# Kernel optimization log

Measured on AMD Instinct MI355X. Metric: run time of the kernel, lower is better.

Reference implementation:

```python
import jax, jax.numpy as jnp
import numpy as np

N, E, F_IN, HID, G, HEADS = 50000, 300000, 128, 256, 1000, 1
NUM_GC, ALPHA = 5, 0.5
EPS_LN = 1e-5
EPS_BN = 1e-5


def _layer_norm(h, g, b):
    m = h.mean(-1, keepdims=True)
    v = jnp.mean((h - m) ** 2, axis=-1, keepdims=True)
    return (h - m) * jax.lax.rsqrt(v + EPS_LN) * g + b


def _l2_normalize_rows(h):
    # F.normalize(h, dim=1)
    n = jnp.sqrt(jnp.sum(h * h, axis=1, keepdims=True))
    return h / jnp.maximum(n, 1e-12)


def full_attention_conv(qs, ks, vs):
    # qs:[N,H,M] ks:[L,H,M] vs:[L,H,D]; global (Frobenius) norm as in torch.norm(p=2)
    qs = qs / jnp.linalg.norm(qs)
    ks = ks / jnp.linalg.norm(ks)
    n = qs.shape[0]
    kvs = jnp.einsum('lhm,lhd->hmd', ks, vs)                 # [H,M,D]
    attn_num = jnp.einsum('nhm,hmd->nhd', qs, kvs) + n * vs  # [N,H,D]
    ks_sum = ks.sum(axis=0)                                  # [H,M]
    norm = jnp.einsum('nhm,hm->nh', qs, ks_sum)[..., None] + n
    return attn_num / norm                                   # [N,H,D]


def setup_inputs() -> dict:
    key = jax.random.key(0)
    ks = jax.random.split(key, 24)
    f32 = jnp.float32

    def lin(k, fan_in, shape):
        return jax.random.normal(k, shape, f32) / np.sqrt(fan_in)

    inp = {}
    inp['x'] = jax.random.normal(ks[0], (N, F_IN), f32)
    inp['edge_index'] = jax.random.randint(ks[1], (2, E), 0, N)
    inp['batch'] = jnp.sort(jax.random.randint(ks[2], (N,), 0, G))
    inp['beta'] = 1
    # TransConv params
    inp['fc_W'] = lin(ks[3], F_IN, (F_IN, HID)); inp['fc_b'] = jnp.zeros((HID,), f32)
    inp['ln0_g'] = jnp.ones((HID,), f32); inp['ln0_b'] = jnp.zeros((HID,), f32)
    inp['Wq'] = lin(ks[4], HID, (HID, HID * HEADS)); inp['bq'] = jnp.zeros((HID * HEADS,), f32)
    inp['Wk'] = lin(ks[5], HID, (HID, HID * HEADS)); inp['bk'] = jnp.zeros((HID * HEADS,), f32)
    inp['Wv'] = lin(ks[6], HID, (HID, HID * HEADS)); inp['bv'] = jnp.zeros((HID * HEADS,), f32)
    inp['ln1_g'] = jnp.ones((HID,), f32); inp['ln1_b'] = jnp.zeros((HID,), f32)
    # GCN stack params
    inp['gcn_W0'] = lin(ks[7], F_IN, (F_IN, HID)); inp['gcn_b0'] = jnp.zeros((HID,), f32)
    inp['gcn_W'] = jnp.stack([lin(ks[8 + i], HID, (HID, HID)) for i in range(NUM_GC - 1)])
    inp['gcn_b'] = jnp.zeros((NUM_GC - 1, HID), f32)
    inp['bn_g'] = jnp.ones((NUM_GC, HID), f32); inp['bn_b'] = jnp.zeros((NUM_GC, HID), f32)
    inp['bn_mean'] = jnp.zeros((NUM_GC, HID), f32); inp['bn_var'] = jnp.ones((NUM_GC, HID), f32)
    return inp


def reference(x, edge_index, batch, beta, fc_W, fc_b, ln0_g, ln0_b,
              Wq, bq, Wk, bk, Wv, bv, ln1_g, ln1_b,
              gcn_W0, gcn_b0, gcn_W, gcn_b, bn_g, bn_b, bn_mean, bn_var):
    n = x.shape[0]
    # ---- TransConv branch (eval mode: dropout = identity) ----
    h = jax.nn.relu(_layer_norm(x @ fc_W + fc_b, ln0_g, ln0_b))
    qs = (h @ Wq + bq).reshape(n, HEADS, HID)
    kk = (h @ Wk + bk).reshape(n, HEADS, HID)
    vv = (h @ Wv + bv).reshape(n, HEADS, HID)
    attn = full_attention_conv(qs, kk, vv).mean(axis=1)      # [N,HID]
    h1 = ALPHA * attn + (1.0 - ALPHA) * h                    # residual
    h1 = jax.nn.relu(_layer_norm(h1, ln1_g, ln1_b))
    x_trans = _l2_normalize_rows(h1)
    # ---- GCN stack ----
    src, dst = edge_index[0], edge_index[1]
    loop = jnp.arange(n)
    src_f = jnp.concatenate([src, loop])
    dst_f = jnp.concatenate([dst, loop])
    deg = jax.ops.segment_sum(jnp.ones_like(src_f, dtype=x.dtype), dst_f, num_segments=n)
    dinv = jax.lax.rsqrt(deg)  # deg >= 1 due to self loops
    enorm = (dinv[src_f] * dinv[dst_f])[:, None]             # [E+N,1]
    g = x
    for i in range(NUM_GC):
        W = gcn_W0 if i == 0 else gcn_W[i - 1]
        b = gcn_b0 if i == 0 else gcn_b[i - 1]
        gw = g @ W
        g = jax.ops.segment_sum(gw[src_f] * enorm, dst_f, num_segments=n) + b
        g = (g - bn_mean[i]) * jax.lax.rsqrt(bn_var[i] + EPS_BN) * bn_g[i] + bn_b[i]
        if i != NUM_GC - 1:
            g = jax.nn.relu(g)
    g = _l2_normalize_rows(g)
    xpool = jax.ops.segment_sum(g, batch, num_segments=G)    # global_add_pool
    return (xpool, g, x_trans)
```

## Files before the change

### kernel.cpp

```cpp
#include <hip/hip_runtime.h>
#include <stdint.h>

#define NN 50000
#define NEDGE 300000
#define FIN 128
#define HID 256
#define NG 1000
#define NLAYER 5

typedef __bf16 bf16x8 __attribute__((ext_vector_type(8)));
typedef float f32x4 __attribute__((ext_vector_type(4)));

__device__ __forceinline__ float us2f(unsigned short u){
  union{ unsigned int i; float f; } c; c.i = ((unsigned int)u) << 16; return c.f;
}
__device__ __forceinline__ unsigned short f2us(float f){
  union{ float f; unsigned int i; } c; c.f = f;
  unsigned int r = c.i + 0x7fff + ((c.i >> 16) & 1);
  return (unsigned short)(r >> 16);
}

__device__ __forceinline__ void gload16(const void* g, void* l){
  __builtin_amdgcn_global_load_lds((__attribute__((address_space(1))) void*)g,
                                   (__attribute__((address_space(3))) void*)l, 16, 0, 0);
}

__device__ __forceinline__ void fma8(float* a, uint4 u, float w){
  a[0] += w * us2f((unsigned short)(u.x & 0xffff));
  a[1] += w * us2f((unsigned short)(u.x >> 16));
  a[2] += w * us2f((unsigned short)(u.y & 0xffff));
  a[3] += w * us2f((unsigned short)(u.y >> 16));
  a[4] += w * us2f((unsigned short)(u.z & 0xffff));
  a[5] += w * us2f((unsigned short)(u.z >> 16));
  a[6] += w * us2f((unsigned short)(u.w & 0xffff));
  a[7] += w * us2f((unsigned short)(u.w >> 16));
}

template<int K, int EPI>
__global__ void gemm_epi(const unsigned short* __restrict__ A,
                         const unsigned short* __restrict__ Wt,
                         const float* __restrict__ bias,
                         const float* __restrict__ p1,
                         const float* __restrict__ p2,
                         const unsigned short* __restrict__ hres,
                         void* __restrict__ outv, int nrows)
{
  __shared__ __align__(16) char smem[20480];
  unsigned short* Alds = (unsigned short*)smem;
  unsigned short* Wlds = (unsigned short*)(smem + 4096);
  const int t = threadIdx.x;
  const int lane = t & 63, w = t >> 6;
  const int r0 = blockIdx.x * 64;

  const int ccl = (t & 3) ^ ((t >> 3) & 3);
  int arow = r0 + (t >> 2); if (arow > nrows - 1) arow = nrows - 1;
  const unsigned short* aSrc = A + (size_t)arow * K + ccl * 8;
  const unsigned short* wSrc[4];
#pragma unroll
  for (int i = 0; i < 4; ++i){
    int c = i * 64 + (t >> 2);
    wSrc[i] = Wt + (size_t)c * K + ccl * 8;
  }

  f32x4 acc[4][4] = {};
  const int lg = lane >> 4, lr = lane & 15;

  for (int k0 = 0; k0 < K; k0 += 32){
    gload16(aSrc + k0, smem + t * 16);
#pragma unroll
    for (int i = 0; i < 4; ++i)
      gload16(wSrc[i] + k0, smem + 4096 + (i * 256 + t) * 16);
    __syncthreads();

    bf16x8 af[4], bfr[4];
#pragma unroll
    for (int mi = 0; mi < 4; ++mi){
      int r = mi * 16 + lr;
      int cp = lg ^ ((r >> 1) & 3);
      af[mi] = *(const bf16x8*)(Alds + (r * 4 + cp) * 8);
    }
#pragma unroll
    for (int ni = 0; ni < 4; ++ni){
      int c = w * 64 + ni * 16 + lr;
      int cp = lg ^ ((c >> 1) & 3);
      bfr[ni] = *(const bf16x8*)(Wlds + (c * 4 + cp) * 8);
    }
#pragma unroll
    for (int mi = 0; mi < 4; ++mi)
#pragma unroll
      for (int ni = 0; ni < 4; ++ni)
        acc[mi][ni] = __builtin_amdgcn_mfma_f32_16x16x32_bf16(af[mi], bfr[ni], acc[mi][ni], 0, 0, 0);
    __syncthreads();
  }

  float g1[4], g2[4], bc[4];
#pragma unroll
  for (int ni = 0; ni < 4; ++ni){
    int c = w * 64 + ni * 16 + lr;
    g1[ni] = p1[c]; g2[ni] = p2[c];
    if (EPI <= 2) bc[ni] = bias[c];
  }

  float* redS = (float*)smem;
  float* redQ = redS + 256;
  float* meanr = redQ + 256;
  float* rstdr = meanr + 64;
  float* invr  = rstdr + 64;

  if (EPI == 1 || EPI == 2){
#pragma unroll
    for (int mi = 0; mi < 4; ++mi)
#pragma unroll
      for (int ni = 0; ni < 4; ++ni)
#pragma unroll
        for (int e = 0; e < 4; ++e){
          float v = acc[mi][ni][e] + bc[ni];
          if (EPI == 2){
            int gr = r0 + mi * 16 + lg * 4 + e; if (gr > nrows - 1) gr = nrows - 1;
            int c = w * 64 + ni * 16 + lr;
            v = 0.5f * v + 0.5f * us2f(hres[(size_t)gr * 256 + c]);
          }
          acc[mi][ni][e] = v;
        }
    float ps[4][4], pq[4][4];
#pragma unroll
    for (int mi = 0; mi < 4; ++mi)
#pragma unroll
      for (int e = 0; e < 4; ++e){
        float s = 0.f, q = 0.f;
#pragma unroll
        for (int ni = 0; ni < 4; ++ni){ float v = acc[mi][ni][e]; s += v; q += v * v; }
        ps[mi][e] = s; pq[mi][e] = q;
      }
#pragma unroll
    for (int m = 1; m <= 8; m <<= 1)
#pragma unroll
      for (int mi = 0; mi < 4; ++mi)
#pragma unroll
        for (int e = 0; e < 4; ++e){
          ps[mi][e] += __shfl_xor(ps[mi][e], m);
          pq[mi][e] += __shfl_xor(pq[mi][e], m);
        }
    if (lr == 0){
#pragma unroll
      for (int mi = 0; mi < 4; ++mi)
#pragma unroll
        for (int e = 0; e < 4; ++e){
          int row = mi * 16 + lg * 4 + e;
          redS[w * 64 + row] = ps[mi][e];
          redQ[w * 64 + row] = pq[mi][e];
        }
    }
    __syncthreads();
    if (t < 64){
      float S = redS[t] + redS[64 + t] + redS[128 + t] + redS[192 + t];
      float Q = redQ[t] + redQ[64 + t] + redQ[128 + t] + redQ[192 + t];
      float mean = S * (1.f / 256.f);
      float var = Q * (1.f / 256.f) - mean * mean;
      meanr[t] = mean; rstdr[t] = rsqrtf(var + 1e-5f);
    }
    __syncthreads();
#pragma unroll
    for (int mi = 0; mi < 4; ++mi)
#pragma unroll
      for (int e = 0; e < 4; ++e){
        int row = mi * 16 + lg * 4 + e;
        float mean = meanr[row], rstd = rstdr[row];
#pragma unroll
        for (int ni = 0; ni < 4; ++ni){
          float y = (acc[mi][ni][e] - mean) * rstd * g1[ni] + g2[ni];
          acc[mi][ni][e] = fmaxf(y, 0.f);
        }
      }
  } else {
#pragma unroll
    for (int mi = 0; mi < 4; ++mi)
#pragma unroll
      for (int ni = 0; ni < 4; ++ni)
#pragma unroll
        for (int e = 0; e < 4; ++e){
          float y = acc[mi][ni][e] * g1[ni] + g2[ni];
          if (EPI == 3) y = fmaxf(y, 0.f);
          acc[mi][ni][e] = y;
        }
  }

  if (EPI == 1 || EPI == 3){
    unsigned short* out = (unsigned short*)outv;
#pragma unroll
    for (int mi = 0; mi < 4; ++mi)
#pragma unroll
      for (int e = 0; e < 4; ++e){
        int gr = r0 + mi * 16 + lg * 4 + e;
        if (gr < nrows){
          unsigned short* orow = out + (size_t)gr * 256 + w * 64 + lr;
#pragma unroll
          for (int ni = 0; ni < 4; ++ni)
            orow[ni * 16] = f2us(acc[mi][ni][e]);
        }
      }
  } else {
    float ps[4][4];
#pragma unroll
    for (int mi = 0; mi < 4; ++mi)
#pragma unroll
      for (int e = 0; e < 4; ++e){
        float s = 0.f;
#pragma unroll
        for (int ni = 0; ni < 4; ++ni){ float v = acc[mi][ni][e]; s += v * v; }
        ps[mi][e] = s;
      }
#pragma unroll
    for (int m = 1; m <= 8; m <<= 1)
#pragma unroll
      for (int mi = 0; mi < 4; ++mi)
#pragma unroll
        for (int e = 0; e < 4; ++e)
          ps[mi][e] += __shfl_xor(ps[mi][e], m);
    __syncthreads();
    if (lr == 0){
#pragma unroll
      for (int mi = 0; mi < 4; ++mi)
#pragma unroll
        for (int e = 0; e < 4; ++e)
          redS[w * 64 + mi * 16 + lg * 4 + e] = ps[mi][e];
    }
    __syncthreads();
    if (t < 64){
      float S = redS[t] + redS[64 + t] + redS[128 + t] + redS[192 + t];
      invr[t] = 1.f / fmaxf(sqrtf(S), 1e-12f);
    }
    __syncthreads();
    float* out = (float*)outv;
#pragma unroll
    for (int mi = 0; mi < 4; ++mi)
#pragma unroll
      for (int e = 0; e < 4; ++e){
        int row = mi * 16 + lg * 4 + e;
        int gr = r0 + row;
        float inv = invr[row];
        if (gr < nrows){
          float* orow = out + (size_t)gr * 256 + w * 64 + lr;
#pragma unroll
          for (int ni = 0; ni < 4; ++ni)
            orow[ni * 16] = acc[mi][ni][e] * inv;
        }
      }
  }
}

__global__ void k_cvt(const float* __restrict__ s, unsigned short* __restrict__ d, int n8){
  int i = blockIdx.x * 256 + threadIdx.x;
  if (i < n8){
    const float4* sp = (const float4*)s + (size_t)i * 2;
    float4 a = sp[0], b = sp[1];
    ushort4 u0, u1;
    u0.x = f2us(a.x); u0.y = f2us(a.y); u0.z = f2us(a.z); u0.w = f2us(a.w);
    u1.x = f2us(b.x); u1.y = f2us(b.y); u1.z = f2us(b.z); u1.w = f2us(b.w);
    ushort4* dp = (ushort4*)d + (size_t)i * 2;
    dp[0] = u0; dp[1] = u1;
  }
}

__global__ void k_wprep(const float* __restrict__ fcW, const float* __restrict__ Wv,
                        const float* __restrict__ gW0, const float* __restrict__ gW,
                        unsigned short* __restrict__ fcWt, unsigned short* __restrict__ WvT,
                        unsigned short* __restrict__ g0T, unsigned short* __restrict__ gWT)
{
  int which = blockIdx.z;
  const float* src; unsigned short* dst; int K;
  if (which == 0){ src = fcW; dst = fcWt; K = FIN; }
  else if (which == 1){ src = Wv; dst = WvT; K = 256; }
  else if (which == 2){ src = gW0; dst = g0T; K = FIN; }
  else { src = gW + (size_t)(which - 3) * 65536; dst = gWT + (size_t)(which - 3) * 65536; K = 256; }
  int bx = blockIdx.x * 64; if (bx >= K) return;
  int by = blockIdx.y * 64;
  __shared__ unsigned short tile[64][65];
  int t = threadIdx.x;
#pragma unroll
  for (int j = 0; j < 16; ++j){
    int idx = j * 256 + t;
    int r = idx >> 6, c = idx & 63;
    tile[r][c] = f2us(src[(size_t)(bx + r) * 256 + by + c]);
  }
  __syncthreads();
#pragma unroll
  for (int j = 0; j < 16; ++j){
    int idx = j * 256 + t;
    int rr = idx >> 6, cc = idx & 63;
    dst[(size_t)(by + rr) * K + bx + cc] = tile[cc][rr];
  }
}

__global__ void k_bnprep(const float* __restrict__ gb0, const float* __restrict__ gb,
                         const float* __restrict__ bng, const float* __restrict__ bnb,
                         const float* __restrict__ bnm, const float* __restrict__ bnv,
                         float* __restrict__ scale, float* __restrict__ shift)
{
  int l = blockIdx.x, c = threadIdx.x;
  int i = l * 256 + c;
  float b = (l == 0) ? gb0[c] : gb[(l - 1) * 256 + c];
  float sc = bng[i] * rsqrtf(bnv[i] + 1e-5f);
  scale[i] = sc;
  shift[i] = (b - bnm[i]) * sc + bnb[i];
}

__global__ void k_deg_init(int* deg){ int i = blockIdx.x * 256 + threadIdx.x; if (i < NN) deg[i] = 1; }
__global__ void k_deg_count(const int* __restrict__ ei, int* deg){
  int e = blockIdx.x * 256 + threadIdx.x;
  if (e < NEDGE) atomicAdd(&deg[ei[NEDGE + e]], 1);
}
__global__ void k_scan_part(const int* __restrict__ deg, int* rp, int* bsum){
  __shared__ int sh[256];
  int t = threadIdx.x, i = blockIdx.x * 256 + t;
  int v = (i < NN) ? deg[i] : 0;
  sh[t] = v; __syncthreads();
  for (int off = 1; off < 256; off <<= 1){
    int x = (t >= off) ? sh[t - off] : 0;
    __syncthreads(); sh[t] += x; __syncthreads();
  }
  if (i < NN) rp[i] = sh[t] - v;
  if (t == 255) bsum[blockIdx.x] = sh[255];
}
__global__ void k_scan_sums(int* rp, int* bsum, int nb){
  __shared__ int sh[256];
  int t = threadIdx.x;
  int v = (t < nb) ? bsum[t] : 0;
  sh[t] = v; __syncthreads();
  for (int off = 1; off < 256; off <<= 1){
    int x = (t >= off) ? sh[t - off] : 0;
    __syncthreads(); sh[t] += x; __syncthreads();
  }
  if (t < nb) bsum[t] = sh[t] - v;
  if (t == 0) rp[NN] = sh[255];
}
__global__ void k_scan_add(int* rp, const int* __restrict__ bsum, const int* __restrict__ deg,
                           int* fill, float* dinv){
  int i = blockIdx.x * 256 + threadIdx.x;
  if (i < NN){
    int r = rp[i] + bsum[i >> 8];
    rp[i] = r; fill[i] = r;
    dinv[i] = rsqrtf((float)deg[i]);
  }
}
__global__ void k_fill_edges(const int* __restrict__ ei, int* fill, int* colx, float* ew,
                             const float* __restrict__ dinv){
  int e = blockIdx.x * 256 + threadIdx.x;
  if (e < NEDGE){
    int s = ei[e], d = ei[NEDGE + e];
    int p = atomicAdd(&fill[d], 1);
    colx[p] = s; ew[p] = dinv[s] * dinv[d];
  }
}
__global__ void k_fill_self(int* fill, int* colx, float* ew, const float* __restrict__ dinv){
  int i = blockIdx.x * 256 + threadIdx.x;
  if (i < NN){
    int p = atomicAdd(&fill[i], 1);
    colx[p] = i; ew[p] = dinv[i] * dinv[i];
  }
}

template<int NC>
__global__ void __launch_bounds__(256) k_aggregate(
    const unsigned short* __restrict__ gsrc, const int* __restrict__ rp,
    const int* __restrict__ colx, const float* __restrict__ ew,
    unsigned short* __restrict__ gout)
{
  constexpr int LG = (NC == 256) ? 5 : 4;
  int tid = blockIdx.x * 256 + threadIdx.x;
  int nd = tid >> LG;
  if (nd >= NN) return;
  int c0 = (tid & ((1 << LG) - 1)) * 8;
  const unsigned short* base = gsrc + c0;
  int jb = rp[nd], je = rp[nd + 1];
  float a0[8] = {}, a1[8] = {};
  int j = jb;
  for (; j + 2 <= je; j += 2){
    int s0 = colx[j], s1 = colx[j + 1];
    float w0 = ew[j], w1 = ew[j + 1];
    uint4 u0 = *(const uint4*)(base + (size_t)s0 * NC);
    uint4 u1 = *(const uint4*)(base + (size_t)s1 * NC);
    fma8(a0, u0, w0);
    fma8(a1, u1, w1);
  }
  if (j < je){
    uint4 u = *(const uint4*)(base + (size_t)colx[j] * NC);
    fma8(a0, u, ew[j]);
  }
  uint4 pk;
  pk.x = (unsigned int)f2us(a0[0] + a1[0]) | ((unsigned int)f2us(a0[1] + a1[1]) << 16);
  pk.y = (unsigned int)f2us(a0[2] + a1[2]) | ((unsigned int)f2us(a0[3] + a1[3]) << 16);
  pk.z = (unsigned int)f2us(a0[4] + a1[4]) | ((unsigned int)f2us(a0[5] + a1[5]) << 16);
  pk.w = (unsigned int)f2us(a0[6] + a1[6]) | ((unsigned int)f2us(a0[7] + a1[7]) << 16);
  *(uint4*)(gout + (size_t)nd * NC + c0) = pk;
}

__global__ void k_gbounds(const int* __restrict__ batch, int* __restrict__ gstart)
{
  int i = blockIdx.x * 256 + threadIdx.x;
  if (i >= NN) return;
  int bc = batch[i];
  int bp = (i == 0) ? -1 : batch[i - 1];
  for (int g = bp + 1; g <= bc; ++g) gstart[g] = i;
  if (i == NN - 1)
    for (int g = bc + 1; g <= NG; ++g) gstart[g] = NN;
}

__global__ void k_pool(const float* __restrict__ out1, const int* __restrict__ gstart,
                       float* __restrict__ out0)
{
  int g = blockIdx.x, c = threadIdx.x;
  int js = gstart[g], je = gstart[g + 1];
  float acc = 0.f;
  int r = js;
  for (; r + 4 <= je; r += 4){
    float a = out1[(size_t)r * 256 + c];
    float b = out1[(size_t)(r + 1) * 256 + c];
    float d = out1[(size_t)(r + 2) * 256 + c];
    float e = out1[(size_t)(r + 3) * 256 + c];
    acc += (a + b) + (d + e);
  }
  for (; r < je; ++r) acc += out1[(size_t)r * 256 + c];
  out0[(size_t)g * 256 + c] = acc;
}

extern "C" void kernel_launch(void* const* d_in, const int* in_sizes, int n_in,
                              void* d_out, int out_size, void* d_ws, size_t ws_size,
                              hipStream_t stream)
{
  const float* x    = (const float*)d_in[0];
  const int*  ei    = (const int*)d_in[1];
  const int*  batch = (const int*)d_in[2];
  const float* fcW  = (const float*)d_in[4];
  const float* fcb  = (const float*)d_in[5];
  const float* ln0g = (const float*)d_in[6];
  const float* ln0b = (const float*)d_in[7];
  const float* Wv   = (const float*)d_in[12];
  const float* bv   = (const float*)d_in[13];
  const float* ln1g = (const float*)d_in[14];
  const float* ln1b = (const float*)d_in[15];
  const float* gW0  = (const float*)d_in[16];
  const float* gb0  = (const float*)d_in[17];
  const float* gW   = (const float*)d_in[18];
  const float* gb   = (const float*)d_in[19];
  const float* bng  = (const float*)d_in[20];
  const float* bnb  = (const float*)d_in[21];
  const float* bnm  = (const float*)d_in[22];
  const float* bnv  = (const float*)d_in[23];

  char* ws = (char*)d_ws;
  unsigned short* xb   = (unsigned short*)(ws);
  unsigned short* hb   = (unsigned short*)(ws + 12800000);
  unsigned short* ga   = (unsigned short*)(ws + 38400000);
  unsigned short* fcWt = (unsigned short*)(ws + 64000000);
  unsigned short* WvT  = (unsigned short*)(ws + 64065536);
  unsigned short* g0T  = (unsigned short*)(ws + 64196608);
  unsigned short* gWT  = (unsigned short*)(ws + 64262144);
  float* bnscale       = (float*)(ws + 64786432);
  float* bnshift       = (float*)(ws + 64791552);
  int*   deg           = (int*)(ws + 64796672);
  int*   rp            = (int*)(ws + 64996672);
  int*   fill          = (int*)(ws + 65196736);
  float* dinv          = (float*)(ws + 65396736);
  int*   colx          = (int*)(ws + 65596736);
  float* ew            = (float*)(ws + 66996736);
  int*   bsum          = (int*)(ws + 68396736);
  int*   gstart        = (int*)(ws + 68397760);

  float* out0 = (float*)d_out;
  float* out1 = out0 + NG * 256;
  float* out2 = out1 + NN * 256;

  k_cvt<<<(NN * FIN / 8 + 255) / 256, 256, 0, stream>>>(x, xb, NN * FIN / 8);
  k_wprep<<<dim3(4, 4, 7), 256, 0, stream>>>(fcW, Wv, gW0, gW, fcWt, WvT, g0T, gWT);
  k_bnprep<<<NLAYER, 256, 0, stream>>>(gb0, gb, bng, bnb, bnm, bnv, bnscale, bnshift);
  k_gbounds<<<196, 256, 0, stream>>>(batch, gstart);

  const int GB = (NN + 63) / 64;
  gemm_epi<FIN, 1><<<GB, 256, 0, stream>>>(xb, fcWt, fcb, ln0g, ln0b, nullptr, hb, NN);
  gemm_epi<256, 2><<<GB, 256, 0, stream>>>(hb, WvT, bv, ln1g, ln1b, hb, out2, NN);

  k_deg_init<<<196, 256, 0, stream>>>(deg);
  k_deg_count<<<(NEDGE + 255) / 256, 256, 0, stream>>>(ei, deg);
  k_scan_part<<<196, 256, 0, stream>>>(deg, rp, bsum);
  k_scan_sums<<<1, 256, 0, stream>>>(rp, bsum, 196);
  k_scan_add<<<196, 256, 0, stream>>>(rp, bsum, deg, fill, dinv);
  k_fill_edges<<<(NEDGE + 255) / 256, 256, 0, stream>>>(ei, fill, colx, ew, dinv);
  k_fill_self<<<196, 256, 0, stream>>>(fill, colx, ew, dinv);

  const int AB128 = (NN * 16 + 255) / 256;
  const int AB256 = (NN * 32 + 255) / 256;
  k_aggregate<128><<<AB128, 256, 0, stream>>>(xb, rp, colx, ew, ga);
  gemm_epi<FIN, 3><<<GB, 256, 0, stream>>>(ga, g0T, nullptr, bnscale, bnshift, nullptr, hb, NN);
  for (int i = 1; i < NLAYER - 1; ++i){
    k_aggregate<256><<<AB256, 256, 0, stream>>>(hb, rp, colx, ew, ga);
    gemm_epi<256, 3><<<GB, 256, 0, stream>>>(ga, gWT + (size_t)(i - 1) * 65536, nullptr,
        bnscale + i * 256, bnshift + i * 256, nullptr, hb, NN);
  }
  k_aggregate<256><<<AB256, 256, 0, stream>>>(hb, rp, colx, ew, ga);
  gemm_epi<256, 4><<<GB, 256, 0, stream>>>(ga, gWT + (size_t)3 * 65536, nullptr,
      bnscale + 4 * 256, bnshift + 4 * 256, nullptr, out1, NN);

  k_pool<<<NG, 256, 0, stream>>>(out1, gstart, out0);
}
```

Measured before the change: 358.2 us.

## Merge preprocessing kernels into one launch and single-block CSR scan

Folds the input conversion, weight transpose, batchnorm folding, graph-bounds and degree-count kernels into one multi-role kernel, replaces the three-kernel prefix scan with a single 1024-thread block, and merges the edge and self-loop fill into one kernel. The degree array is zeroed with a memset and the self-loop +1 is added during the scan. The goal is to cut about ten kernel launches and their serialization gaps. The trade-off is that the single-block scan runs serially over about 49 elements per thread.

```diff
diff --git a/kernel.cpp b/kernel.cpp
--- a/kernel.cpp
+++ b/kernel.cpp
@@ -249,114 +249,129 @@
   }
 }
 
-__global__ void k_cvt(const float* __restrict__ s, unsigned short* __restrict__ d, int n8){
-  int i = blockIdx.x * 256 + threadIdx.x;
-  if (i < n8){
-    const float4* sp = (const float4*)s + (size_t)i * 2;
-    float4 a = sp[0], b = sp[1];
+#define PB_CVT 3125
+#define PB_WP  112
+#define PB_BN  NLAYER
+#define PB_GB  196
+#define PB_DC  1172
+#define PB_TOTAL (PB_CVT + PB_WP + PB_BN + PB_GB + PB_DC)
+
+__global__ void k_pre(const float* __restrict__ x, unsigned short* __restrict__ xb,
+                      const float* __restrict__ fcW, const float* __restrict__ Wv,
+                      const float* __restrict__ gW0, const float* __restrict__ gW,
+                      unsigned short* __restrict__ fcWt, unsigned short* __restrict__ WvT,
+                      unsigned short* __restrict__ g0T, unsigned short* __restrict__ gWT,
+                      const float* __restrict__ gb0, const float* __restrict__ gb,
+                      const float* __restrict__ bng, const float* __restrict__ bnb,
+                      const float* __restrict__ bnm, const float* __restrict__ bnv,
+                      float* __restrict__ bnscale, float* __restrict__ bnshift,
+                      const int* __restrict__ batch, int* __restrict__ gstart,
+                      const int* __restrict__ ei, int* __restrict__ deg)
+{
+  __shared__ unsigned short tile[64][65];
+  int b = blockIdx.x, t = threadIdx.x;
+  if (b < PB_CVT){
+    int i = b * 256 + t;
+    const float4* sp = (const float4*)x + (size_t)i * 2;
+    float4 a = sp[0], bb = sp[1];
     ushort4 u0, u1;
     u0.x = f2us(a.x); u0.y = f2us(a.y); u0.z = f2us(a.z); u0.w = f2us(a.w);
-    u1.x = f2us(b.x); u1.y = f2us(b.y); u1.z = f2us(b.z); u1.w = f2us(b.w);
-    ushort4* dp = (ushort4*)d + (size_t)i * 2;
+    u1.x = f2us(bb.x); u1.y = f2us(bb.y); u1.z = f2us(bb.z); u1.w = f2us(bb.w);
+    ushort4* dp = (ushort4*)xb + (size_t)i * 2;
     dp[0] = u0; dp[1] = u1;
-  }
-}
-
-__global__ void k_wprep(const float* __restrict__ fcW, const float* __restrict__ Wv,
-                        const float* __restrict__ gW0, const float* __restrict__ gW,
-                        unsigned short* __restrict__ fcWt, unsigned short* __restrict__ WvT,
-                        unsigned short* __restrict__ g0T, unsigned short* __restrict__ gWT)
-{
-  int which = blockIdx.z;
-  const float* src; unsigned short* dst; int K;
-  if (which == 0){ src = fcW; dst = fcWt; K = FIN; }
-  else if (which == 1){ src = Wv; dst = WvT; K = 256; }
-  else if (which == 2){ src = gW0; dst = g0T; K = FIN; }
-  else { src = gW + (size_t)(which - 3) * 65536; dst = gWT + (size_t)(which - 3) * 65536; K = 256; }
-  int bx = blockIdx.x * 64; if (bx >= K) return;
-  int by = blockIdx.y * 64;
-  __shared__ unsigned short tile[64][65];
+    return;
+  }
+  b -= PB_CVT;
+  if (b < PB_WP){
+    int which = b >> 4, r = b & 15;
+    const float* src; unsigned short* dst; int K;
+    if (which == 0){ src = fcW; dst = fcWt; K = FIN; }
+    else if (which == 1){ src = Wv; dst = WvT; K = 256; }
+    else if (which == 2){ src = gW0; dst = g0T; K = FIN; }
+    else { src = gW + (size_t)(which - 3) * 65536; dst = gWT + (size_t)(which - 3) * 65536; K = 256; }
+    int bx = (r & 3) * 64; if (bx >= K) return;
+    int by = (r >> 2) * 64;
+#pragma unroll
+    for (int j = 0; j < 16; ++j){
+      int idx = j * 256 + t;
+      int rr = idx >> 6, cc = idx & 63;
+      tile[rr][cc] = f2us(src[(size_t)(bx + rr) * 256 + by + cc]);
+    }
+    __syncthreads();
+#pragma unroll
+    for (int j = 0; j < 16; ++j){
+      int idx = j * 256 + t;
+      int rr = idx >> 6, cc = idx & 63;
+      dst[(size_t)(by + rr) * K + bx + cc] = tile[cc][rr];
+    }
+    return;
+  }
+  b -= PB_WP;
+  if (b < PB_BN){
+    int i = b * 256 + t;
+    float bias = (b == 0) ? gb0[t] : gb[(b - 1) * 256 + t];
+    float sc = bng[i] * rsqrtf(bnv[i] + 1e-5f);
+    bnscale[i] = sc;
+    bnshift[i] = (bias - bnm[i]) * sc + bnb[i];
+    return;
+  }
+  b -= PB_BN;
+  if (b < PB_GB){
+    int i = b * 256 + t;
+    if (i >= NN) return;
+    int bc = batch[i];
+    int bp = (i == 0) ? -1 : batch[i - 1];
+    for (int g = bp + 1; g <= bc; ++g) gstart[g] = i;
+    if (i == NN - 1)
+      for (int g = bc + 1; g <= NG; ++g) gstart[g] = NN;
+    return;
+  }
+  b -= PB_GB;
+  {
+    int e = b * 256 + t;
+    if (e < NEDGE) atomicAdd(&deg[ei[NEDGE + e]], 1);
+  }
+}
+
+__global__ void __launch_bounds__(1024) k_scan_one(
+    const int* __restrict__ deg, int* __restrict__ rp,
+    int* __restrict__ fill, float* __restrict__ dinv)
+{
+  __shared__ int sh[1024];
   int t = threadIdx.x;
-#pragma unroll
-  for (int j = 0; j < 16; ++j){
-    int idx = j * 256 + t;
-    int r = idx >> 6, c = idx & 63;
-    tile[r][c] = f2us(src[(size_t)(bx + r) * 256 + by + c]);
-  }
-  __syncthreads();
-#pragma unroll
-  for (int j = 0; j < 16; ++j){
-    int idx = j * 256 + t;
-    int rr = idx >> 6, cc = idx & 63;
-    dst[(size_t)(by + rr) * K + bx + cc] = tile[cc][rr];
-  }
-}
-
-__global__ void k_bnprep(const float* __restrict__ gb0, const float* __restrict__ gb,
-                         const float* __restrict__ bng, const float* __restrict__ bnb,
-                         const float* __restrict__ bnm, const float* __restrict__ bnv,
-                         float* __restrict__ scale, float* __restrict__ shift)
-{
-  int l = blockIdx.x, c = threadIdx.x;
-  int i = l * 256 + c;
-  float b = (l == 0) ? gb0[c] : gb[(l - 1) * 256 + c];
-  float sc = bng[i] * rsqrtf(bnv[i] + 1e-5f);
-  scale[i] = sc;
-  shift[i] = (b - bnm[i]) * sc + bnb[i];
-}
-
-__global__ void k_deg_init(int* deg){ int i = blockIdx.x * 256 + threadIdx.x; if (i < NN) deg[i] = 1; }
-__global__ void k_deg_count(const int* __restrict__ ei, int* deg){
-  int e = blockIdx.x * 256 + threadIdx.x;
-  if (e < NEDGE) atomicAdd(&deg[ei[NEDGE + e]], 1);
-}
-__global__ void k_scan_part(const int* __restrict__ deg, int* rp, int* bsum){
-  __shared__ int sh[256];
-  int t = threadIdx.x, i = blockIdx.x * 256 + t;
-  int v = (i < NN) ? deg[i] : 0;
-  sh[t] = v; __syncthreads();
-  for (int off = 1; off < 256; off <<= 1){
-    int x = (t >= off) ? sh[t - off] : 0;
-    __syncthreads(); sh[t] += x; __syncthreads();
-  }
-  if (i < NN) rp[i] = sh[t] - v;
-  if (t == 255) bsum[blockIdx.x] = sh[255];
-}
-__global__ void k_scan_sums(int* rp, int* bsum, int nb){
-  __shared__ int sh[256];
-  int t = threadIdx.x;
-  int v = (t < nb) ? bsum[t] : 0;
-  sh[t] = v; __syncthreads();
-  for (int off = 1; off < 256; off <<= 1){
-    int x = (t >= off) ? sh[t - off] : 0;
-    __syncthreads(); sh[t] += x; __syncthreads();
-  }
-  if (t < nb) bsum[t] = sh[t] - v;
-  if (t == 0) rp[NN] = sh[255];
-}
-__global__ void k_scan_add(int* rp, const int* __restrict__ bsum, const int* __restrict__ deg,
-                           int* fill, float* dinv){
-  int i = blockIdx.x * 256 + threadIdx.x;
-  if (i < NN){
-    int r = rp[i] + bsum[i >> 8];
-    rp[i] = r; fill[i] = r;
-    dinv[i] = rsqrtf((float)deg[i]);
-  }
-}
-__global__ void k_fill_edges(const int* __restrict__ ei, int* fill, int* colx, float* ew,
-                             const float* __restrict__ dinv){
+  const int per = (NN + 1023) / 1024;
+  int s = t * per, e = s + per; if (e > NN) e = NN; if (s > NN) s = NN;
+  int sum = 0;
+  for (int i = s; i < e; ++i) sum += deg[i] + 1;
+  sh[t] = sum; __syncthreads();
+  for (int off = 1; off < 1024; off <<= 1){
+    int v = (t >= off) ? sh[t - off] : 0;
+    __syncthreads(); sh[t] += v; __syncthreads();
+  }
+  int base = sh[t] - sum;
+  for (int i = s; i < e; ++i){
+    int d = deg[i] + 1;
+    rp[i] = base; fill[i] = base;
+    dinv[i] = rsqrtf((float)d);
+    base += d;
+  }
+  if (t == 1023) rp[NN] = sh[1023];
+}
+
+__global__ void k_fill(const int* __restrict__ ei, int* __restrict__ fill,
+                       int* __restrict__ colx, float* __restrict__ ew,
+                       const float* __restrict__ dinv)
+{
   int e = blockIdx.x * 256 + threadIdx.x;
   if (e < NEDGE){
     int s = ei[e], d = ei[NEDGE + e];
     int p = atomicAdd(&fill[d], 1);
     colx[p] = s; ew[p] = dinv[s] * dinv[d];
-  }
-}
-__global__ void k_fill_self(int* fill, int* colx, float* ew, const float* __restrict__ dinv){
-  int i = blockIdx.x * 256 + threadIdx.x;
-  if (i < NN){
+  } else if (e < NEDGE + NN){
+    int i = e - NEDGE;
     int p = atomicAdd(&fill[i], 1);
-    colx[p] = i; ew[p] = dinv[i] * dinv[i];
+    float di = dinv[i];
+    colx[p] = i; ew[p] = di * di;
   }
 }
 
@@ -393,17 +408,6 @@
   pk.z = (unsigned int)f2us(a0[4] + a1[4]) | ((unsigned int)f2us(a0[5] + a1[5]) << 16);
   pk.w = (unsigned int)f2us(a0[6] + a1[6]) | ((unsigned int)f2us(a0[7] + a1[7]) << 16);
   *(uint4*)(gout + (size_t)nd * NC + c0) = pk;
-}
-
-__global__ void k_gbounds(const int* __restrict__ batch, int* __restrict__ gstart)
-{
-  int i = blockIdx.x * 256 + threadIdx.x;
-  if (i >= NN) return;
-  int bc = batch[i];
-  int bp = (i == 0) ? -1 : batch[i - 1];
-  for (int g = bp + 1; g <= bc; ++g) gstart[g] = i;
-  if (i == NN - 1)
-    for (int g = bc + 1; g <= NG; ++g) gstart[g] = NN;
 }
 
 __global__ void k_pool(const float* __restrict__ out1, const int* __restrict__ gstart,
@@ -464,29 +468,22 @@
   float* dinv          = (float*)(ws + 65396736);
   int*   colx          = (int*)(ws + 65596736);
   float* ew            = (float*)(ws + 66996736);
-  int*   bsum          = (int*)(ws + 68396736);
-  int*   gstart        = (int*)(ws + 68397760);
+  int*   gstart        = (int*)(ws + 68396736);
 
   float* out0 = (float*)d_out;
   float* out1 = out0 + NG * 256;
   float* out2 = out1 + NN * 256;
 
-  k_cvt<<<(NN * FIN / 8 + 255) / 256, 256, 0, stream>>>(x, xb, NN * FIN / 8);
-  k_wprep<<<dim3(4, 4, 7), 256, 0, stream>>>(fcW, Wv, gW0, gW, fcWt, WvT, g0T, gWT);
-  k_bnprep<<<NLAYER, 256, 0, stream>>>(gb0, gb, bng, bnb, bnm, bnv, bnscale, bnshift);
-  k_gbounds<<<196, 256, 0, stream>>>(batch, gstart);
+  hipMemsetAsync(deg, 0, NN * sizeof(int), stream);
+  k_pre<<<PB_TOTAL, 256, 0, stream>>>(x, xb, fcW, Wv, gW0, gW, fcWt, WvT, g0T, gWT,
+                                      gb0, gb, bng, bnb, bnm, bnv, bnscale, bnshift,
+                                      batch, gstart, ei, deg);
+  k_scan_one<<<1, 1024, 0, stream>>>(deg, rp, fill, dinv);
+  k_fill<<<(NEDGE + NN + 255) / 256, 256, 0, stream>>>(ei, fill, colx, ew, dinv);
 
   const int GB = (NN + 63) / 64;
   gemm_epi<FIN, 1><<<GB, 256, 0, stream>>>(xb, fcWt, fcb, ln0g, ln0b, nullptr, hb, NN);
   gemm_epi<256, 2><<<GB, 256, 0, stream>>>(hb, WvT, bv, ln1g, ln1b, hb, out2, NN);
-
-  k_deg_init<<<196, 256, 0, stream>>>(deg);
-  k_deg_count<<<(NEDGE + 255) / 256, 256, 0, stream>>>(ei, deg);
-  k_scan_part<<<196, 256, 0, stream>>>(deg, rp, bsum);
-  k_scan_sums<<<1, 256, 0, stream>>>(rp, bsum, 196);
-  k_scan_add<<<196, 256, 0, stream>>>(rp, bsum, deg, fill, dinv);
-  k_fill_edges<<<(NEDGE + 255) / 256, 256, 0, stream>>>(ei, fill, colx, ew, dinv);
-  k_fill_self<<<196, 256, 0, stream>>>(fill, colx, ew, dinv);
 
   const int AB128 = (NN * 16 + 255) / 256;
   const int AB256 = (NN * 32 + 255) / 256;
```

New measurement: 475.7 us. +32.8%, slower.
